# Kernel tuning notes

Hardware: AMD Instinct MI355X
Metric: run time of the kernel (lower is better)

The kernel has to match this reference:

```python
import jax, jax.numpy as jnp
import numpy as np


def _lstm_scan(x_tbd, Wih, Whh, bih, bhh):
    """Standard LSTM cell (PyTorch i,f,g,o gate order) scanned over time.
    x_tbd: [T,B,D]; returns hidden states [T,B,H]."""
    H = Whh.shape[1]
    B = x_tbd.shape[1]

    def step(carry, x_t):
        h, c = carry
        gates = x_t @ Wih.T + bih + h @ Whh.T + bhh  # [B,4H]
        i, f, g, o = jnp.split(gates, 4, axis=-1)
        c = jax.nn.sigmoid(f) * c + jax.nn.sigmoid(i) * jnp.tanh(g)
        h = jax.nn.sigmoid(o) * jnp.tanh(c)
        return (h, c), h

    h0 = jnp.zeros((B, H), x_tbd.dtype)
    _, hs = jax.lax.scan(step, (h0, h0), x_tbd)
    return hs


def setup_inputs() -> dict:
    key = jax.random.key(0)
    B, T, D, H = 64, 1024, 512, 256  # output_dim=1024 -> H = output_dim//4 per direction
    ks = jax.random.split(key, 9)
    s = 0.05
    mk = lambda k, shape: jax.random.normal(k, shape, jnp.float32) * s
    return {
        "input": mk(ks[0], (B, T, D)),
        "Wih_f": mk(ks[1], (4 * H, D)), "Whh_f": mk(ks[2], (4 * H, H)),
        "bih_f": mk(ks[3], (4 * H,)),   "bhh_f": mk(ks[4], (4 * H,)),
        "Wih_b": mk(ks[5], (4 * H, D)), "Whh_b": mk(ks[6], (4 * H, H)),
        "bih_b": mk(ks[7], (4 * H,)),   "bhh_b": mk(ks[8], (4 * H,)),
    }


def reference(input, Wih_f, Whh_f, bih_f, bhh_f, Wih_b, Whh_b, bih_b, bhh_b):
    # [B,T,D] -> [T,B,D] for scan over time
    x_tbd = jnp.transpose(input, (1, 0, 2))
    hf = _lstm_scan(x_tbd, Wih_f, Whh_f, bih_f, bhh_f)            # forward in time
    hb = _lstm_scan(x_tbd[::-1], Wih_b, Whh_b, bih_b, bhh_b)[::-1]  # backward, re-aligned
    # output[t] = cat(outputf[t], outputb[T-1-t]) == cat(hf[t], hb_aligned[t])
    out = jnp.concatenate([hf, hb], axis=-1)  # [T,B,2H]
    return jnp.transpose(out, (1, 0, 2))      # [B,T,2H]
```

## Files before the change

### kernel.cpp

```cpp
#include <hip/hip_runtime.h>
#include <hip/hip_bf16.h>

typedef __attribute__((ext_vector_type(8))) short bf8;
typedef __attribute__((ext_vector_type(4))) float f32x4;

#define T_SEQ 1024

__device__ __forceinline__ float sigm(float x) { return 1.f / (1.f + __expf(-x)); }
__device__ __forceinline__ float tanh_(float x) { return 2.f / (1.f + __expf(-2.f * x)) - 1.f; }

__device__ __forceinline__ short bf16s(float x) {
    union { __hip_bfloat16 h; short s; } u;
    u.h = __float2bfloat16(x);
    return u.s;
}

__device__ __forceinline__ bf8 pack_bf8(const float4 a, const float4 b) {
    bf8 r;
    r[0] = bf16s(a.x); r[1] = bf16s(a.y); r[2] = bf16s(a.z); r[3] = bf16s(a.w);
    r[4] = bf16s(b.x); r[5] = bf16s(b.y); r[6] = bf16s(b.z); r[7] = bf16s(b.w);
    return r;
}

__global__ __launch_bounds__(256) void xproj_kernel(
    const float* __restrict__ X,
    const float* __restrict__ WihF,
    const float* __restrict__ bihF,
    const float* __restrict__ bhhF,
    const float* __restrict__ WihB,
    const float* __restrict__ bihB,
    const float* __restrict__ bhhB,
    __hip_bfloat16* __restrict__ XpF,
    __hip_bfloat16* __restrict__ XpB)
{
    const int dir = blockIdx.z;
    const float* W  = dir ? WihB : WihF;
    const float* bi = dir ? bihB : bihF;
    const float* bh = dir ? bhhB : bhhF;
    __hip_bfloat16* Xp = dir ? XpB : XpF;

    __shared__ __align__(16) short As[128 * 32];
    __shared__ __align__(16) short Bs[128 * 32];

    const int tid  = threadIdx.x;
    const int lane = tid & 63;
    const int w    = tid >> 6;
    const int quad = lane >> 4;
    const int l16  = lane & 15;
    const int wr   = w >> 1, wc = w & 1;

    const int m0 = blockIdx.x * 128;
    const int n0 = blockIdx.y * 128;

    const int srow = tid >> 2;
    const int scg  = tid & 3;

    f32x4 acc[4][4] = {};

    for (int kk = 0; kk < 512; kk += 32) {
        const float* pa0 = X + (size_t)(m0 + srow)      * 512 + kk + scg * 8;
        const float* pa1 = X + (size_t)(m0 + 64 + srow) * 512 + kk + scg * 8;
        const float* pb0 = W + (size_t)(n0 + srow)      * 512 + kk + scg * 8;
        const float* pb1 = W + (size_t)(n0 + 64 + srow) * 512 + kk + scg * 8;
        bf8 a0 = pack_bf8(*(const float4*)pa0, *(const float4*)(pa0 + 4));
        bf8 a1 = pack_bf8(*(const float4*)pa1, *(const float4*)(pa1 + 4));
        bf8 b0 = pack_bf8(*(const float4*)pb0, *(const float4*)(pb0 + 4));
        bf8 b1 = pack_bf8(*(const float4*)pb1, *(const float4*)(pb1 + 4));
        __syncthreads();
        *(bf8*)&As[(srow)      * 32 + scg * 8] = a0;
        *(bf8*)&As[(64 + srow) * 32 + scg * 8] = a1;
        *(bf8*)&Bs[(srow)      * 32 + scg * 8] = b0;
        *(bf8*)&Bs[(64 + srow) * 32 + scg * 8] = b1;
        __syncthreads();

        bf8 af[4], bfr[4];
#pragma unroll
        for (int mt = 0; mt < 4; mt++)
            af[mt] = *(const bf8*)&As[(wr * 64 + mt * 16 + l16) * 32 + quad * 8];
#pragma unroll
        for (int nt = 0; nt < 4; nt++)
            bfr[nt] = *(const bf8*)&Bs[(wc * 64 + nt * 16 + l16) * 32 + quad * 8];
#pragma unroll
        for (int mt = 0; mt < 4; mt++)
#pragma unroll
            for (int nt = 0; nt < 4; nt++)
                acc[mt][nt] = __builtin_amdgcn_mfma_f32_16x16x32_bf16(af[mt], bfr[nt], acc[mt][nt], 0, 0, 0);
    }

#pragma unroll
    for (int nt = 0; nt < 4; nt++) {
        const int n = n0 + wc * 64 + nt * 16 + l16;
        const float bias = bi[n] + bh[n];
#pragma unroll
        for (int mt = 0; mt < 4; mt++) {
#pragma unroll
            for (int r = 0; r < 4; r++) {
                const int m = m0 + wr * 64 + mt * 16 + quad * 4 + r;
                const int b = m >> 10, t = m & 1023;
                Xp[((size_t)t * 64 + b) * 1024 + n] = __float2bfloat16(acc[mt][nt][r] + bias);
            }
        }
    }
}

__global__ __launch_bounds__(256, 1) void lstm_rec_kernel(
    const __hip_bfloat16* __restrict__ XpF,
    const __hip_bfloat16* __restrict__ XpB,
    const float* __restrict__ WhhF,
    const float* __restrict__ WhhB,
    __hip_bfloat16* __restrict__ hexch,
    int* __restrict__ flags,
    float* __restrict__ out)
{
    const int wg  = blockIdx.x;
    const int dir = wg >> 4;
    const int s   = wg & 15;
    const int tid  = threadIdx.x;
    const int lane = tid & 63;
    const int w    = tid >> 6;
    const int quad = lane >> 4;
    const int l16  = lane & 15;

    const __hip_bfloat16* Xp = dir ? XpB : XpF;
    const float* Whh         = dir ? WhhB : WhhF;
    unsigned int* hexchU     = (unsigned int*)hexch;

    __shared__ unsigned int hstage[512];

    bf8 Bf[4][8];
#pragma unroll
    for (int g = 0; g < 4; g++)
#pragma unroll
        for (int k = 0; k < 8; k++) {
            const float* p = Whh + (size_t)(g * 256 + s * 16 + l16) * 256 + k * 32 + quad * 8;
            Bf[g][k] = pack_bf8(*(const float4*)p, *(const float4*)(p + 4));
        }

    float c[4] = {0.f, 0.f, 0.f, 0.f};

    {
        unsigned int* slice0 = hexchU + ((size_t)(0 * 2 + dir) * 16 + s) * 512;
        for (int i = tid; i < 512; i += 256)
            __hip_atomic_store(&slice0[i], 0u, __ATOMIC_RELAXED, __HIP_MEMORY_SCOPE_AGENT);
    }
    __syncthreads();
    if (tid == 0)
        __hip_atomic_store(&flags[(dir * 16 + s) * 16], 0, __ATOMIC_RELEASE, __HIP_MEMORY_SCOPE_AGENT);

    for (int tau = 0; tau < T_SEQ; tau++) {
        const int t = dir ? (T_SEQ - 1 - tau) : tau;

        float xp[4][4];
#pragma unroll
        for (int g = 0; g < 4; g++)
#pragma unroll
            for (int r = 0; r < 4; r++) {
                const int b = w * 16 + quad * 4 + r;
                xp[g][r] = __bfloat162float(Xp[((size_t)t * 64 + b) * 1024 + g * 256 + s * 16 + l16]);
            }

        if (tid < 16) {
            const int fidx = (dir * 16 + tid) * 16;
            while (__hip_atomic_load(&flags[fidx], __ATOMIC_RELAXED, __HIP_MEMORY_SCOPE_AGENT) < tau)
                __builtin_amdgcn_s_sleep(1);
        }
        __syncthreads();
        __builtin_amdgcn_fence(__ATOMIC_ACQUIRE, "agent");

        const __hip_bfloat16* hb = hexch + ((size_t)((tau & 1) * 2 + dir) * 16) * 1024;
        bf8 Af[8];
#pragma unroll
        for (int k = 0; k < 8; k++) {
            const int sA = k * 2 + (quad >> 1);
            Af[k] = *(const bf8*)(hb + (size_t)sA * 1024 + (w * 16 + l16) * 16 + (quad & 1) * 8);
        }

        f32x4 acc[4];
#pragma unroll
        for (int g = 0; g < 4; g++) { f32x4 a = {xp[g][0], xp[g][1], xp[g][2], xp[g][3]}; acc[g] = a; }
#pragma unroll
        for (int k = 0; k < 8; k++)
#pragma unroll
            for (int g = 0; g < 4; g++)
                acc[g] = __builtin_amdgcn_mfma_f32_16x16x32_bf16(Af[k], Bf[g][k], acc[g], 0, 0, 0);

        float hv[4];
#pragma unroll
        for (int r = 0; r < 4; r++) {
            const float ig = sigm(acc[0][r]);
            const float fg = sigm(acc[1][r]);
            const float gg = tanh_(acc[2][r]);
            const float og = sigm(acc[3][r]);
            c[r] = fg * c[r] + ig * gg;
            hv[r] = og * tanh_(c[r]);
            const int b = w * 16 + quad * 4 + r;
            ((__hip_bfloat16*)hstage)[b * 16 + l16] = __float2bfloat16(hv[r]);
        }
        __syncthreads();

        {
            unsigned int* dst = hexchU + ((size_t)(((tau + 1) & 1) * 2 + dir) * 16 + s) * 512;
            __hip_atomic_store(&dst[2 * tid],     hstage[2 * tid],     __ATOMIC_RELAXED, __HIP_MEMORY_SCOPE_AGENT);
            __hip_atomic_store(&dst[2 * tid + 1], hstage[2 * tid + 1], __ATOMIC_RELAXED, __HIP_MEMORY_SCOPE_AGENT);
        }
        __syncthreads();
        if (tid == 0)
            __hip_atomic_store(&flags[(dir * 16 + s) * 16], tau + 1, __ATOMIC_RELEASE, __HIP_MEMORY_SCOPE_AGENT);

#pragma unroll
        for (int r = 0; r < 4; r++) {
            const int b = w * 16 + quad * 4 + r;
            __builtin_nontemporal_store(hv[r], &out[((size_t)b * T_SEQ + t) * 512 + dir * 256 + s * 16 + l16]);
        }
    }
}

extern "C" void kernel_launch(void* const* d_in, const int* in_sizes, int n_in,
                              void* d_out, int out_size, void* d_ws, size_t ws_size,
                              hipStream_t stream)
{
    const float* X    = (const float*)d_in[0];
    const float* WihF = (const float*)d_in[1];
    const float* WhhF = (const float*)d_in[2];
    const float* bihF = (const float*)d_in[3];
    const float* bhhF = (const float*)d_in[4];
    const float* WihB = (const float*)d_in[5];
    const float* WhhB = (const float*)d_in[6];
    const float* bihB = (const float*)d_in[7];
    const float* bhhB = (const float*)d_in[8];
    float* out = (float*)d_out;

    char* ws = (char*)d_ws;
    __hip_bfloat16* XpF   = (__hip_bfloat16*)ws;
    __hip_bfloat16* XpB   = (__hip_bfloat16*)(ws + 134217728);
    __hip_bfloat16* hexch = (__hip_bfloat16*)(ws + 268435456);
    int*            flags = (int*)(ws + 268435456 + 131072);

    dim3 g1(512, 8, 2);
    xproj_kernel<<<g1, 256, 0, stream>>>(X, WihF, bihF, bhhF, WihB, bihB, bhhB, XpF, XpB);
    lstm_rec_kernel<<<32, 256, 0, stream>>>(XpF, XpB, WhhF, WhhB, hexch, flags, out);
}
```

Before: 4.661 ms.

## Replace atomic flag sync with sc1 inline-asm loads/stores and busy-wait spin

```diff
diff --git a/kernel.cpp b/kernel.cpp
--- a/kernel.cpp
+++ b/kernel.cpp
@@ -3,6 +3,7 @@
 
 typedef __attribute__((ext_vector_type(8))) short bf8;
 typedef __attribute__((ext_vector_type(4))) float f32x4;
+typedef __attribute__((ext_vector_type(2))) unsigned int u32x2;
 
 #define T_SEQ 1024
 
@@ -20,6 +21,32 @@
     r[0] = bf16s(a.x); r[1] = bf16s(a.y); r[2] = bf16s(a.z); r[3] = bf16s(a.w);
     r[4] = bf16s(b.x); r[5] = bf16s(b.y); r[6] = bf16s(b.z); r[7] = bf16s(b.w);
     return r;
+}
+
+__device__ __forceinline__ void store_sc1_b64(void* p, unsigned int lo, unsigned int hi) {
+    u32x2 v; v[0] = lo; v[1] = hi;
+    asm volatile("global_store_dwordx2 %0, %1, off sc1" :: "v"(p), "v"(v) : "memory");
+}
+__device__ __forceinline__ void store_sc1_b32(void* p, unsigned int v) {
+    asm volatile("global_store_dword %0, %1, off sc1" :: "v"(p), "v"(v) : "memory");
+}
+__device__ __forceinline__ unsigned int load_sc1_b32(const void* p) {
+    unsigned int v;
+    asm volatile("global_load_dword %0, %1, off sc1\n"
+                 "s_waitcnt vmcnt(0)"
+                 : "=v"(v) : "v"(p) : "memory");
+    return v;
+}
+__device__ __forceinline__ bf8 load_sc1_b128(const void* p) {
+    bf8 v;
+    asm volatile("global_load_dwordx4 %0, %1, off sc1" : "=v"(v) : "v"(p) : "memory");
+    return v;
+}
+
+__global__ __launch_bounds__(256) void init_kernel(unsigned int* __restrict__ p, int n)
+{
+    const int i = blockIdx.x * 256 + threadIdx.x;
+    if (i < n) p[i] = 0u;
 }
 
 __global__ __launch_bounds__(256) void xproj_kernel(
@@ -138,46 +165,40 @@
 
     float c[4] = {0.f, 0.f, 0.f, 0.f};
 
-    {
-        unsigned int* slice0 = hexchU + ((size_t)(0 * 2 + dir) * 16 + s) * 512;
-        for (int i = tid; i < 512; i += 256)
-            __hip_atomic_store(&slice0[i], 0u, __ATOMIC_RELAXED, __HIP_MEMORY_SCOPE_AGENT);
-    }
-    __syncthreads();
-    if (tid == 0)
-        __hip_atomic_store(&flags[(dir * 16 + s) * 16], 0, __ATOMIC_RELEASE, __HIP_MEMORY_SCOPE_AGENT);
 
     for (int tau = 0; tau < T_SEQ; tau++) {
         const int t = dir ? (T_SEQ - 1 - tau) : tau;
 
-        float xp[4][4];
+        if (tid < 16) {
+            int* f = &flags[(dir * 16 + tid) * 32];
+            while ((int)load_sc1_b32(f) < tau) { }
+        }
+        __syncthreads();
+
+        unsigned short xpu[4][4];
 #pragma unroll
         for (int g = 0; g < 4; g++)
 #pragma unroll
             for (int r = 0; r < 4; r++) {
                 const int b = w * 16 + quad * 4 + r;
-                xp[g][r] = __bfloat162float(Xp[((size_t)t * 64 + b) * 1024 + g * 256 + s * 16 + l16]);
+                xpu[g][r] = __builtin_nontemporal_load(
+                    (const unsigned short*)&Xp[((size_t)t * 64 + b) * 1024 + g * 256 + s * 16 + l16]);
             }
-
-        if (tid < 16) {
-            const int fidx = (dir * 16 + tid) * 16;
-            while (__hip_atomic_load(&flags[fidx], __ATOMIC_RELAXED, __HIP_MEMORY_SCOPE_AGENT) < tau)
-                __builtin_amdgcn_s_sleep(1);
-        }
-        __syncthreads();
-        __builtin_amdgcn_fence(__ATOMIC_ACQUIRE, "agent");
 
         const __hip_bfloat16* hb = hexch + ((size_t)((tau & 1) * 2 + dir) * 16) * 1024;
         bf8 Af[8];
 #pragma unroll
         for (int k = 0; k < 8; k++) {
             const int sA = k * 2 + (quad >> 1);
-            Af[k] = *(const bf8*)(hb + (size_t)sA * 1024 + (w * 16 + l16) * 16 + (quad & 1) * 8);
-        }
+            Af[k] = load_sc1_b128(hb + (size_t)sA * 1024 + (w * 16 + l16) * 16 + (quad & 1) * 8);
+        }
+        asm volatile("s_waitcnt vmcnt(0)" ::: "memory");
+        __builtin_amdgcn_sched_barrier(0);
 
         f32x4 acc[4];
-#pragma unroll
-        for (int g = 0; g < 4; g++) { f32x4 a = {xp[g][0], xp[g][1], xp[g][2], xp[g][3]}; acc[g] = a; }
+        const f32x4 zero = {0.f, 0.f, 0.f, 0.f};
+#pragma unroll
+        for (int g = 0; g < 4; g++) acc[g] = zero;
 #pragma unroll
         for (int k = 0; k < 8; k++)
 #pragma unroll
@@ -187,10 +208,15 @@
         float hv[4];
 #pragma unroll
         for (int r = 0; r < 4; r++) {
-            const float ig = sigm(acc[0][r]);
-            const float fg = sigm(acc[1][r]);
-            const float gg = tanh_(acc[2][r]);
-            const float og = sigm(acc[3][r]);
+            union { unsigned int u; float f; } cv0, cv1, cv2, cv3;
+            cv0.u = (unsigned int)xpu[0][r] << 16;
+            cv1.u = (unsigned int)xpu[1][r] << 16;
+            cv2.u = (unsigned int)xpu[2][r] << 16;
+            cv3.u = (unsigned int)xpu[3][r] << 16;
+            const float ig = sigm(acc[0][r] + cv0.f);
+            const float fg = sigm(acc[1][r] + cv1.f);
+            const float gg = tanh_(acc[2][r] + cv2.f);
+            const float og = sigm(acc[3][r] + cv3.f);
             c[r] = fg * c[r] + ig * gg;
             hv[r] = og * tanh_(c[r]);
             const int b = w * 16 + quad * 4 + r;
@@ -200,12 +226,12 @@
 
         {
             unsigned int* dst = hexchU + ((size_t)(((tau + 1) & 1) * 2 + dir) * 16 + s) * 512;
-            __hip_atomic_store(&dst[2 * tid],     hstage[2 * tid],     __ATOMIC_RELAXED, __HIP_MEMORY_SCOPE_AGENT);
-            __hip_atomic_store(&dst[2 * tid + 1], hstage[2 * tid + 1], __ATOMIC_RELAXED, __HIP_MEMORY_SCOPE_AGENT);
-        }
+            store_sc1_b64(&dst[2 * tid], hstage[2 * tid], hstage[2 * tid + 1]);
+        }
+        asm volatile("s_waitcnt vmcnt(0)" ::: "memory");
         __syncthreads();
         if (tid == 0)
-            __hip_atomic_store(&flags[(dir * 16 + s) * 16], tau + 1, __ATOMIC_RELEASE, __HIP_MEMORY_SCOPE_AGENT);
+            store_sc1_b32(&flags[(dir * 16 + s) * 32], (unsigned int)(tau + 1));
 
 #pragma unroll
         for (int r = 0; r < 4; r++) {
@@ -236,6 +262,9 @@
     __hip_bfloat16* hexch = (__hip_bfloat16*)(ws + 268435456);
     int*            flags = (int*)(ws + 268435456 + 131072);
 
+    const int initN = (131072 + 4096) / 4;
+    init_kernel<<<(initN + 255) / 256, 256, 0, stream>>>((unsigned int*)(ws + 268435456), initN);
+
     dim3 g1(512, 8, 2);
     xproj_kernel<<<g1, 256, 0, stream>>>(X, WihF, bihF, bhhF, WihB, bihB, bhhB, XpF, XpB);
     lstm_rec_kernel<<<32, 256, 0, stream>>>(XpF, XpB, WhhF, WhhB, hexch, flags, out);
```

Result: faster. 4.364 ms (median of 2 runs) (-6.4%).
